# Kernel optimization log

Hardware: AMD Instinct MI355X
Metric: run time of the kernel (lower is better)

The kernel has to match this reference:

```python
import jax, jax.numpy as jnp
import numpy as np

B, N, H, OBS, A = 64, 64, 128, 128, 16
TAU = 0.5
BN = B * N
SQRT_H = float(np.sqrt(H))
_ar = np.arange(N)
# off-diagonal gather indices: row i lists all j != i in increasing order,
# matching torch's eye-mask boolean select in row-major order
IDX = jnp.asarray(np.stack([np.concatenate([_ar[:i], _ar[i + 1:]]) for i in range(N)]))  # [N, N-1]


def setup_inputs() -> dict:
    key = jax.random.key(0)
    ks = jax.random.split(key, 26)
    w = lambda k, s: jax.random.normal(k, s, jnp.float32) * 0.05
    return {
        "obs": jax.random.normal(ks[0], (BN, OBS), jnp.float32),
        "lstm_h": jax.random.normal(ks[1], (BN, 1, H), jnp.float32),
        "lstm_c": jax.random.normal(ks[2], (BN, 1, H), jnp.float32),
        "masks": jnp.ones((BN, 1), jnp.float32),
        "W_enc": w(ks[3], (H, OBS)), "b_enc": jnp.zeros((H,), jnp.float32),
        "lstm_Wih": w(ks[4], (4 * H, H)), "lstm_Whh": w(ks[5], (4 * H, H)),
        "lstm_bih": jnp.zeros((4 * H,), jnp.float32), "lstm_bhh": jnp.zeros((4 * H,), jnp.float32),
        "gru_Wih_f": w(ks[6], (3 * H, 2 * H)), "gru_Whh_f": w(ks[7], (3 * H, H)),
        "gru_bih_f": jnp.zeros((3 * H,), jnp.float32), "gru_bhh_f": jnp.zeros((3 * H,), jnp.float32),
        "gru_Wih_b": w(ks[8], (3 * H, 2 * H)), "gru_Whh_b": w(ks[9], (3 * H, H)),
        "gru_bih_b": jnp.zeros((3 * H,), jnp.float32), "gru_bhh_b": jnp.zeros((3 * H,), jnp.float32),
        "W_hard": w(ks[10], (2, 2 * H)), "b_hard": jnp.zeros((2,), jnp.float32),
        "Wq": w(ks[11], (H, H)), "Wk": w(ks[12], (H, H)),
        "W_act": w(ks[13], (A, 2 * H)), "b_act": jnp.zeros((A,), jnp.float32),
        # fixed Gumbel noise for the gumbel-softmax (makes reference deterministic)
        "gumbel": -jnp.log(-jnp.log(jax.random.uniform(ks[14], (BN, N - 1, 2), jnp.float32, 1e-6, 1.0 - 1e-6))),
    }


def _gru_scan(x_seq, Wih, Whh, bih, bhh):
    # x_seq: [T, BN2, 2H] -> outputs [T, BN2, H]
    def step(hst, x):
        gi = x @ Wih.T + bih
        gh = hst @ Whh.T + bhh
        gi_r, gi_z, gi_n = jnp.split(gi, 3, -1)
        gh_r, gh_z, gh_n = jnp.split(gh, 3, -1)
        r = jax.nn.sigmoid(gi_r + gh_r)
        z = jax.nn.sigmoid(gi_z + gh_z)
        n = jnp.tanh(gi_n + r * gh_n)
        hn = (1.0 - z) * n + z * hst
        return hn, hn
    h0 = jnp.zeros((x_seq.shape[1], Whh.shape[1]), x_seq.dtype)
    _, outs = jax.lax.scan(step, h0, x_seq)
    return outs


def _forward(obs, lstm_h, lstm_c, masks, W_enc, b_enc, lstm_Wih, lstm_Whh, lstm_bih,
             lstm_bhh, gru_Wih_f, gru_Whh_f, gru_bih_f, gru_bhh_f, gru_Wih_b, gru_Whh_b,
             gru_bih_b, gru_bhh_b, W_hard, b_hard, Wq, Wk, W_act, b_act, gumbel):
    # MLP encoder
    h = jax.nn.relu(obs @ W_enc.T + b_enc)                       # [BN, H]
    # single-step LSTM (recurrent_N = 1), mask resets states
    hprev = lstm_h[:, 0] * masks
    cprev = lstm_c[:, 0] * masks
    gates = h @ lstm_Wih.T + lstm_bih + hprev @ lstm_Whh.T + lstm_bhh
    i, f, g, o = jnp.split(gates, 4, -1)
    c_new = jax.nn.sigmoid(f) * cprev + jax.nn.sigmoid(i) * jnp.tanh(g)
    h = jax.nn.sigmoid(o) * jnp.tanh(c_new)                      # [BN, H]
    h_new, c_out = h[:, None, :], c_new[:, None, :]
    hb = h.reshape(B, N, H)
    h_others = hb[:, IDX]                                        # [B, N, N-1, H]
    h_self = jnp.broadcast_to(hb[:, :, None, :], (B, N, N - 1, H))
    h_pair = jnp.concatenate([h_self, h_others], -1).reshape(BN, N - 1, 2 * H)
    # bidirectional GRU over the N-1 "other agents" axis
    xs = jnp.swapaxes(h_pair, 0, 1)                              # [N-1, BN, 2H]
    out_f = _gru_scan(xs, gru_Wih_f, gru_Whh_f, gru_bih_f, gru_bhh_f)
    out_b = _gru_scan(xs[::-1], gru_Wih_b, gru_Whh_b, gru_bih_b, gru_bhh_b)[::-1]
    gru_out = jnp.swapaxes(jnp.concatenate([out_f, out_b], -1), 0, 1)  # [BN, N-1, 2H]
    # hard attention: gumbel-softmax (straight-through), keep channel 1
    logits = gru_out @ W_hard.T + b_hard                         # [BN, N-1, 2]
    y_soft = jax.nn.softmax((logits + gumbel) / TAU, axis=-1)
    y_hard = jax.nn.one_hot(jnp.argmax(y_soft, -1), 2, dtype=y_soft.dtype)
    y = jax.lax.stop_gradient(y_hard - y_soft) + y_soft
    hard_w = y[:, :, 1].reshape(B, N, N - 1, 1)
    # soft attention (manual scaled dot product over other agents)
    q = (h @ Wq.T).reshape(B, N, H)
    k = (h @ Wk.T).reshape(B, N, H)
    k_others = k[:, IDX]                                         # [B, N, N-1, H]
    soft_w = jax.nn.softmax(jnp.einsum('bnh,bnmh->bnm', q, k_others) / SQRT_H, axis=-1)
    x = jnp.sum(h_others * hard_w * soft_w[..., None], axis=2).reshape(BN, H)
    # action head (Discrete, deterministic=True -> argmax)
    act_logits = jnp.concatenate([h, x], -1) @ W_act.T + b_act   # [BN, A]
    logp = jax.nn.log_softmax(act_logits, -1)
    actions = jnp.argmax(act_logits, -1)
    alp = jnp.take_along_axis(logp, actions[:, None], axis=-1)   # [BN, 1]
    return actions[:, None], alp, h_new, c_out


def reference(obs, lstm_h, lstm_c, masks, W_enc, b_enc, lstm_Wih, lstm_Whh, lstm_bih,
              lstm_bhh, gru_Wih_f, gru_Whh_f, gru_bih_f, gru_bhh_f, gru_Wih_b, gru_Whh_b,
              gru_bih_b, gru_bhh_b, W_hard, b_hard, Wq, Wk, W_act, b_act, gumbel):
    return _forward(obs, lstm_h, lstm_c, masks, W_enc, b_enc, lstm_Wih, lstm_Whh,
                    lstm_bih, lstm_bhh, gru_Wih_f, gru_Whh_f, gru_bih_f, gru_bhh_f,
                    gru_Wih_b, gru_Whh_b, gru_bih_b, gru_bhh_b, W_hard, b_hard,
                    Wq, Wk, W_act, b_act, gumbel)
```

## Files before the change

### kernel.cpp

```cpp
#include <hip/hip_runtime.h>
#include <hip/hip_bf16.h>
#include <math.h>

#define BB   64
#define NN   64
#define HH   128
#define OBS_ 128
#define AA   16
#define BN_  4096
#define NM   63
#define G3   384
#define G4   512
#define UVS  1536
#define QKS  256
#define LDSW 136

typedef _Float16 f16x8 __attribute__((ext_vector_type(8)));
typedef float    f32x4 __attribute__((ext_vector_type(4)));

__device__ __forceinline__ float fsig(float x) {
    return __builtin_amdgcn_rcpf(1.0f + __builtin_amdgcn_exp2f(-1.4426950408889634f * x));
}
__device__ __forceinline__ float ftanh(float x) {
    return 1.0f - 2.0f * __builtin_amdgcn_rcpf(1.0f + __builtin_amdgcn_exp2f(2.8853900817779268f * x));
}

__device__ __forceinline__ unsigned short h2u(_Float16 h) {
    union { _Float16 f; unsigned short u; } cv; cv.f = h; return cv.u;
}

template<bool DUAL, bool RELU, bool RMASK>
__global__ __launch_bounds__(256)
void gemm_mfma(const float* __restrict__ A, int lda,
               const float* __restrict__ A2, int lda2,
               const float* __restrict__ rmask,
               const float* __restrict__ Bs0, const float* __restrict__ Bs1,
               const float* __restrict__ Bs2, const float* __restrict__ Bs3,
               const float* __restrict__ Bd, int ldb, int tilesPerSeg,
               const float* __restrict__ bias0, const float* __restrict__ bias1,
               const float* __restrict__ bias2, const float* __restrict__ bias3,
               float* __restrict__ C, int ldc)
{
    __shared__ __align__(16) unsigned short aHi[64][LDSW];
    __shared__ __align__(16) unsigned short aLo[64][LDSW];

    const int t = threadIdx.x;
    const int w = t >> 6, l = t & 63, li = l & 15, lg = l >> 4;
    const int bx = blockIdx.x, by = blockIdx.y;
    const int seg = bx / tilesPerSeg;
    const int cts = (bx % tilesPerSeg) * 64;
    const float* Bseg    = seg == 0 ? Bs0  : seg == 1 ? Bs1  : seg == 2 ? Bs2  : Bs3;
    const float* biasSeg = seg == 0 ? bias0 : seg == 1 ? bias1 : seg == 2 ? bias2 : bias3;
    const int row0 = by * 64;
    const int cl = w * 16 + li;

    f32x4 accA[4], accB[4];
    #pragma unroll
    for (int rt = 0; rt < 4; ++rt) {
        accA[rt] = (f32x4){0.f,0.f,0.f,0.f};
        accB[rt] = (f32x4){0.f,0.f,0.f,0.f};
    }

    const int npass = DUAL ? 2 : 1;
    for (int pass = 0; pass < npass; ++pass) {
        const float* Ap = pass ? A2 : A;
        const int ldap = pass ? lda2 : lda;
        __syncthreads();
        {
            const int ar = t >> 2, kof = (t & 3) * 32;
            const float* src = Ap + (size_t)(row0 + ar) * ldap + kof;
            float mk = 1.0f;
            if (RMASK && pass == 1) mk = rmask[row0 + ar];
            #pragma unroll
            for (int q = 0; q < 8; ++q) {
                float4 v = *(const float4*)(src + q * 4);
                if (RMASK && pass == 1) { v.x *= mk; v.y *= mk; v.z *= mk; v.w *= mk; }
                float vv[4] = {v.x, v.y, v.z, v.w};
                unsigned int hi01, hi23, lo01, lo23;
                {
                    _Float16 h0 = (_Float16)vv[0], h1 = (_Float16)vv[1];
                    _Float16 h2 = (_Float16)vv[2], h3 = (_Float16)vv[3];
                    _Float16 l0 = (_Float16)((vv[0] - (float)h0) * 1024.0f);
                    _Float16 l1 = (_Float16)((vv[1] - (float)h1) * 1024.0f);
                    _Float16 l2 = (_Float16)((vv[2] - (float)h2) * 1024.0f);
                    _Float16 l3 = (_Float16)((vv[3] - (float)h3) * 1024.0f);
                    hi01 = (unsigned int)h2u(h0) | ((unsigned int)h2u(h1) << 16);
                    hi23 = (unsigned int)h2u(h2) | ((unsigned int)h2u(h3) << 16);
                    lo01 = (unsigned int)h2u(l0) | ((unsigned int)h2u(l1) << 16);
                    lo23 = (unsigned int)h2u(l2) | ((unsigned int)h2u(l3) << 16);
                }
                *(uint2*)&aHi[ar][kof + q * 4] = make_uint2(hi01, hi23);
                *(uint2*)&aLo[ar][kof + q * 4] = make_uint2(lo01, lo23);
            }
        }
        const float* Bp = (DUAL && pass) ? Bd : Bseg;
        f16x8 bhi[4], blo[4];
        #pragma unroll
        for (int kt = 0; kt < 4; ++kt) {
            const float* srcB = Bp + (size_t)(cts + cl) * ldb + kt * 32 + lg * 8;
            #pragma unroll
            for (int j = 0; j < 8; ++j) {
                float wv = srcB[j];
                _Float16 hi = (_Float16)wv;
                _Float16 lo = (_Float16)((wv - (float)hi) * 1024.0f);
                bhi[kt][j] = hi;
                blo[kt][j] = lo;
            }
        }
        __syncthreads();
        #pragma unroll
        for (int kt = 0; kt < 4; ++kt) {
            const int koff = kt * 32 + lg * 8;
            #pragma unroll
            for (int rt = 0; rt < 4; ++rt) {
                f16x8 ah = *(const f16x8*)&aHi[rt * 16 + li][koff];
                f16x8 al = *(const f16x8*)&aLo[rt * 16 + li][koff];
                accA[rt] = __builtin_amdgcn_mfma_f32_16x16x32_f16(ah, bhi[kt], accA[rt], 0, 0, 0);
                accB[rt] = __builtin_amdgcn_mfma_f32_16x16x32_f16(al, bhi[kt], accB[rt], 0, 0, 0);
                accB[rt] = __builtin_amdgcn_mfma_f32_16x16x32_f16(ah, blo[kt], accB[rt], 0, 0, 0);
            }
        }
    }

    const float bv = biasSeg ? biasSeg[cts + cl] : 0.0f;
    const int gcol = bx * 64 + cl;
    #pragma unroll
    for (int rt = 0; rt < 4; ++rt)
        #pragma unroll
        for (int rg = 0; rg < 4; ++rg) {
            float x = fmaf(accB[rt][rg], 9.765625e-4f, accA[rt][rg]) + bv;
            if (RELU) x = fmaxf(x, 0.0f);
            const int r = row0 + rt * 16 + lg * 4 + rg;
            C[(size_t)r * ldc + gcol] = x;
        }
}

__global__ void lstm_pointwise(const float* __restrict__ gates,
                               const float* __restrict__ bih, const float* __restrict__ bhh,
                               const float* __restrict__ lstm_c, const float* __restrict__ masks,
                               float* __restrict__ h,
                               float* __restrict__ out_h, float* __restrict__ out_c)
{
    int idx = blockIdx.x * 256 + threadIdx.x;
    int r = idx >> 7, c = idx & 127;
    const float* g = gates + (size_t)r * G4;
    float gi = g[c]        + bih[c]        + bhh[c];
    float gf = g[128 + c]  + bih[128 + c]  + bhh[128 + c];
    float gg = g[256 + c]  + bih[256 + c]  + bhh[256 + c];
    float go = g[384 + c]  + bih[384 + c]  + bhh[384 + c];
    float cprev = lstm_c[idx] * masks[r];
    float cn = fsig(gf) * cprev + fsig(gi) * ftanh(gg);
    float hn = fsig(go) * ftanh(cn);
    h[idx] = hn;
    out_h[idx] = hn;
    out_c[idx] = cn;
}

__global__ __launch_bounds__(512, 2)
void gru_scan(const float* __restrict__ WhhF, const float* __restrict__ WhhB,
              const float* __restrict__ bhhF, const float* __restrict__ bhhB,
              const float* __restrict__ uv,
              const float* __restrict__ Whard,
              float* __restrict__ partF, float* __restrict__ partB)
{
    __shared__ __align__(16) unsigned short hHi[2][32][LDSW];
    __shared__ __align__(16) unsigned short hLo[2][32][LDSW];
    __shared__ float partLds[32][64][2];

    const int t = threadIdx.x;
    const int dir = blockIdx.x >> 7;
    const int blk = blockIdx.x & 127;
    const int r0 = blk * 32;
    const int bbx = r0 >> 6;
    const int n0 = r0 & 63;
    const int w  = t >> 6;
    const int l  = t & 63;
    const int li = l & 15;
    const int lg = l >> 4;
    const int cl = w * 16 + li;
    const bool pw = (w < 2);

    const float* Whh = dir ? WhhB : WhhF;
    const float* bhh = dir ? bhhB : bhhF;
    const float* U   = uv + dir * 768;
    const float* V   = uv + dir * 768 + 384;
    float* part      = dir ? partB : partF;

    f16x8 Bhi[3][4], Blo[3][4];
    #pragma unroll
    for (int g = 0; g < 3; ++g)
        #pragma unroll
        for (int kt = 0; kt < 4; ++kt) {
            const float* src = Whh + (size_t)(g * 128 + cl) * 128 + kt * 32 + lg * 8;
            #pragma unroll
            for (int j = 0; j < 8; ++j) {
                float wv = src[j];
                _Float16 hi = (_Float16)wv;
                _Float16 lo = (_Float16)((wv - (float)hi) * 1024.0f);
                Bhi[g][kt][j] = hi;
                Blo[g][kt][j] = lo;
            }
        }

    f16x8 Phi[4], Plo[4];
    if (pw) {
        #pragma unroll
        for (int kt = 0; kt < 4; ++kt) {
            #pragma unroll
            for (int j = 0; j < 8; ++j) {
                float wv = (li < 2) ? Whard[li * 256 + dir * 128 + kt * 32 + lg * 8 + j] : 0.0f;
                _Float16 hi = (_Float16)wv;
                _Float16 lo = (_Float16)((wv - (float)hi) * 1024.0f);
                Phi[kt][j] = hi;
                Plo[kt][j] = lo;
            }
        }
    }

    const float bh_r = bhh[cl];
    const float bh_z = bhh[128 + cl];
    const float bh_n = bhh[256 + cl];
    float u_r[8], u_z[8], u_n[8];
    #pragma unroll
    for (int rt = 0; rt < 2; ++rt)
        #pragma unroll
        for (int rg = 0; rg < 4; ++rg) {
            const int idx = rt * 4 + rg;
            const int R = r0 + rt * 16 + lg * 4 + rg;
            const float* Ur = U + (size_t)R * UVS;
            u_r[idx] = Ur[cl]       + bh_r;
            u_z[idx] = Ur[128 + cl] + bh_z;
            u_n[idx] = Ur[256 + cl] + bh_n;
        }

    const int vbase = bbx << 6;
    float v0r, v0z, v0n, v1r, v1z, v1n;
    {
        const int tt0 = dir ? (NM - 1) : 0;
        const float* Vr0 = V + (size_t)(vbase + tt0) * UVS;
        const float* Vr1 = V + (size_t)(vbase + tt0 + 1) * UVS;
        v0r = Vr0[cl]; v0z = Vr0[128 + cl]; v0n = Vr0[256 + cl];
        v1r = Vr1[cl]; v1z = Vr1[128 + cl]; v1n = Vr1[256 + cl];
    }

    for (int i = t; i < 2 * 32 * LDSW; i += 512) {
        (&hHi[0][0][0])[i] = 0;
        (&hLo[0][0][0])[i] = 0;
    }
    float hreg[8] = {0.f,0.f,0.f,0.f,0.f,0.f,0.f,0.f};

    int cur = 0;
    __syncthreads();

    for (int s = 0; s < NM; ++s) {
        const int tt = dir ? (NM - 1 - s) : s;

        float p0r, p0z, p0n, p1r, p1z, p1n;
        {
            const int sn = (s + 1 < NM) ? s + 1 : s;
            const int ttn = dir ? (NM - 1 - sn) : sn;
            const float* Vr0 = V + (size_t)(vbase + ttn) * UVS;
            const float* Vr1 = V + (size_t)(vbase + ttn + 1) * UVS;
            p0r = Vr0[cl]; p0z = Vr0[128 + cl]; p0n = Vr0[256 + cl];
            p1r = Vr1[cl]; p1z = Vr1[128 + cl]; p1n = Vr1[256 + cl];
        }

        f32x4 accA[3][2], accB[3][2], pA, pB;
        #pragma unroll
        for (int g = 0; g < 3; ++g)
            #pragma unroll
            for (int rt = 0; rt < 2; ++rt) {
                accA[g][rt] = (f32x4){0.f,0.f,0.f,0.f};
                accB[g][rt] = (f32x4){0.f,0.f,0.f,0.f};
            }
        pA = pB = (f32x4){0.f,0.f,0.f,0.f};

        #pragma unroll
        for (int kt = 0; kt < 4; ++kt) {
            f16x8 Ahi[2], Alo[2];
            const int koff = kt * 32 + lg * 8;
            #pragma unroll
            for (int rt = 0; rt < 2; ++rt) {
                const int arow = rt * 16 + li;
                Ahi[rt] = *(const f16x8*)&hHi[cur][arow][koff];
                Alo[rt] = *(const f16x8*)&hLo[cur][arow][koff];
            }
            #pragma unroll
            for (int g = 0; g < 3; ++g)
                #pragma unroll
                for (int rt = 0; rt < 2; ++rt) {
                    accA[g][rt] = __builtin_amdgcn_mfma_f32_16x16x32_f16(Ahi[rt], Bhi[g][kt], accA[g][rt], 0, 0, 0);
                    accB[g][rt] = __builtin_amdgcn_mfma_f32_16x16x32_f16(Alo[rt], Bhi[g][kt], accB[g][rt], 0, 0, 0);
                    accB[g][rt] = __builtin_amdgcn_mfma_f32_16x16x32_f16(Ahi[rt], Blo[g][kt], accB[g][rt], 0, 0, 0);
                }
            if (pw) {
                const f16x8 Aph = (w == 0) ? Ahi[0] : Ahi[1];
                const f16x8 Apl = (w == 0) ? Alo[0] : Alo[1];
                pA = __builtin_amdgcn_mfma_f32_16x16x32_f16(Aph, Phi[kt], pA, 0, 0, 0);
                pB = __builtin_amdgcn_mfma_f32_16x16x32_f16(Apl, Phi[kt], pB, 0, 0, 0);
                pB = __builtin_amdgcn_mfma_f32_16x16x32_f16(Aph, Plo[kt], pB, 0, 0, 0);
            }
        }

        if (pw && s > 0 && li < 2) {
            const int ttp = dir ? (tt + 1) : (tt - 1);
            #pragma unroll
            for (int rg = 0; rg < 4; ++rg) {
                const int row = w * 16 + lg * 4 + rg;
                partLds[row][ttp][li] = pA[rg] + pB[rg] * 9.765625e-4f;
            }
        }

        #pragma unroll
        for (int rt = 0; rt < 2; ++rt) {
            #pragma unroll
            for (int rg = 0; rg < 4; ++rg) {
                const int idx = rt * 4 + rg;
                const int row = rt * 16 + lg * 4 + rg;
                const int n = n0 + row;
                const bool up = (tt >= n);
                const float vr_ = up ? v1r : v0r;
                const float vz_ = up ? v1z : v0z;
                const float vn_ = up ? v1n : v0n;
                const float gr = fmaf(accB[0][rt][rg], 9.765625e-4f, accA[0][rt][rg]);
                const float gz = fmaf(accB[1][rt][rg], 9.765625e-4f, accA[1][rt][rg]);
                const float gn = fmaf(accB[2][rt][rg], 9.765625e-4f, accA[2][rt][rg]);
                const float rr  = fsig(u_r[idx] + vr_ + gr);
                const float zz  = fsig(u_z[idx] + vz_ + gz);
                const float nn2 = ftanh(u_n[idx] + vn_ + rr * gn);
                hreg[idx] = fmaf(zz, hreg[idx] - nn2, nn2);
            }
        }

        v0r = p0r; v0z = p0z; v0n = p0n;
        v1r = p1r; v1z = p1z; v1n = p1n;

        const int nxt = cur ^ 1;
        #pragma unroll
        for (int rt = 0; rt < 2; ++rt)
            #pragma unroll
            for (int rg = 0; rg < 4; ++rg) {
                const int row = rt * 16 + lg * 4 + rg;
                const float hn = hreg[rt * 4 + rg];
                _Float16 hi = (_Float16)hn;
                _Float16 lo = (_Float16)((hn - (float)hi) * 1024.0f);
                hHi[nxt][row][cl] = h2u(hi);
                hLo[nxt][row][cl] = h2u(lo);
            }
        cur = nxt;
        __syncthreads();
    }

    if (pw) {
        f32x4 qA = (f32x4){0.f,0.f,0.f,0.f}, qB = (f32x4){0.f,0.f,0.f,0.f};
        #pragma unroll
        for (int kt = 0; kt < 4; ++kt) {
            const int koff = kt * 32 + lg * 8;
            f16x8 Ah = *(const f16x8*)&hHi[cur][w * 16 + li][koff];
            f16x8 Al = *(const f16x8*)&hLo[cur][w * 16 + li][koff];
            qA = __builtin_amdgcn_mfma_f32_16x16x32_f16(Ah, Phi[kt], qA, 0, 0, 0);
            qB = __builtin_amdgcn_mfma_f32_16x16x32_f16(Al, Phi[kt], qB, 0, 0, 0);
            qB = __builtin_amdgcn_mfma_f32_16x16x32_f16(Ah, Plo[kt], qB, 0, 0, 0);
        }
        if (li < 2) {
            const int ttl = dir ? 0 : NM - 1;
            #pragma unroll
            for (int rg = 0; rg < 4; ++rg) {
                const int row = w * 16 + lg * 4 + rg;
                partLds[row][ttl][li] = qA[rg] + qB[rg] * 9.765625e-4f;
            }
        }
    }
    __syncthreads();

    {
        const int row = t >> 4;
        const int seg = t & 15;
        float* dst = part + (size_t)(r0 + row) * (NM * 2);
        #pragma unroll
        for (int k = 0; k < 4; ++k) {
            const int m = seg * 4 + k;
            if (m < NM) {
                float2 v = *(const float2*)&partLds[row][m][0];
                *(float2*)&dst[m * 2] = v;
            }
        }
    }
}

__global__ __launch_bounds__(128)
void attn_final(const float* __restrict__ h, const float* __restrict__ qk,
                const float* __restrict__ partF, const float* __restrict__ partB,
                const float* __restrict__ bhard, const float* __restrict__ gum,
                const float* __restrict__ Wact, const float* __restrict__ bact,
                float* __restrict__ out_act, float* __restrict__ out_alp)
{
    const int r = blockIdx.x;
    const int bbx = r >> 6, n = r & 63;
    const int t = threadIdx.x;
    __shared__ float qsh[HH], wsh[NM], shh[HH], shx[HH];
    if (t < HH) { qsh[t] = qk[(size_t)r * QKS + t]; shh[t] = h[(size_t)r * HH + t]; }
    __syncthreads();
    if (t < 64) {
        float sc = -INFINITY;
        float hardv = 0.0f;
        if (t < NM) {
            const int idxm = t + (t >= n ? 1 : 0);
            const float4* kr = (const float4*)(qk + (size_t)((bbx << 6) + idxm) * QKS + 128);
            float s = 0.0f;
            #pragma unroll
            for (int j4 = 0; j4 < 32; ++j4) {
                float4 kv = kr[j4];
                float4 qv = *(const float4*)&qsh[j4 * 4];
                s += kv.x * qv.x + kv.y * qv.y + kv.z * qv.z + kv.w * qv.w;
            }
            sc = s * 0.088388347648318447f;
            const float2 pf = *(const float2*)(partF + ((size_t)r * NM + t) * 2);
            const float2 pb = *(const float2*)(partB + ((size_t)r * NM + t) * 2);
            const float2 gv = *(const float2*)(gum + ((size_t)r * NM + t) * 2);
            const float l0 = pf.x + pb.x + bhard[0] + gv.x;
            const float l1 = pf.y + pb.y + bhard[1] + gv.y;
            hardv = (l1 > l0) ? 1.0f : 0.0f;
        }
        float mx = sc;
        #pragma unroll
        for (int d = 32; d; d >>= 1) mx = fmaxf(mx, __shfl_xor(mx, d, 64));
        const float e = (t < NM) ? expf(sc - mx) : 0.0f;
        float sum = e;
        #pragma unroll
        for (int d = 32; d; d >>= 1) sum += __shfl_xor(sum, d, 64);
        if (t < NM) wsh[t] = hardv * e / sum;
    }
    __syncthreads();
    {
        const int j = t;
        float x = 0.0f;
        for (int m = 0; m < NM; ++m) {
            const int idxm = m + (m >= n ? 1 : 0);
            x = fmaf(wsh[m], h[(size_t)((bbx << 6) + idxm) * HH + j], x);
        }
        shx[j] = x;
    }
    __syncthreads();
    if (t < 16) {
        const float* wa = Wact + (size_t)t * 256;
        float acc = bact[t];
        #pragma unroll
        for (int j4 = 0; j4 < 32; ++j4) {
            float4 w1 = *(const float4*)&wa[j4 * 4];
            float4 hv = *(const float4*)&shh[j4 * 4];
            float4 w2 = *(const float4*)&wa[128 + j4 * 4];
            float4 xv = *(const float4*)&shx[j4 * 4];
            acc += w1.x * hv.x + w1.y * hv.y + w1.z * hv.z + w1.w * hv.w
                 + w2.x * xv.x + w2.y * xv.y + w2.z * xv.z + w2.w * xv.w;
        }
        float mx = acc; int am = t;
        #pragma unroll
        for (int d = 8; d; d >>= 1) {
            const float om = __shfl_xor(mx, d, 16);
            const int   oa = __shfl_xor(am, d, 16);
            if (om > mx || (om == mx && oa < am)) { mx = om; am = oa; }
        }
        const float e = expf(acc - mx);
        float sum = e;
        #pragma unroll
        for (int d = 8; d; d >>= 1) sum += __shfl_xor(sum, d, 16);
        if (t == 0) {
            out_act[r] = (float)am;
            out_alp[r] = -logf(sum);
        }
    }
}

extern "C" void kernel_launch(void* const* d_in, const int* in_sizes, int n_in,
                              void* d_out, int out_size, void* d_ws, size_t ws_size,
                              hipStream_t stream)
{
    const float* obs    = (const float*)d_in[0];
    const float* lstm_h = (const float*)d_in[1];
    const float* lstm_c = (const float*)d_in[2];
    const float* masks  = (const float*)d_in[3];
    const float* W_enc  = (const float*)d_in[4];
    const float* b_enc  = (const float*)d_in[5];
    const float* lWih   = (const float*)d_in[6];
    const float* lWhh   = (const float*)d_in[7];
    const float* lbih   = (const float*)d_in[8];
    const float* lbhh   = (const float*)d_in[9];
    const float* gWihf  = (const float*)d_in[10];
    const float* gWhhf  = (const float*)d_in[11];
    const float* gbihf  = (const float*)d_in[12];
    const float* gbhhf  = (const float*)d_in[13];
    const float* gWihb  = (const float*)d_in[14];
    const float* gWhhb  = (const float*)d_in[15];
    const float* gbihb  = (const float*)d_in[16];
    const float* gbhhb  = (const float*)d_in[17];
    const float* Whard  = (const float*)d_in[18];
    const float* bhard  = (const float*)d_in[19];
    const float* Wq     = (const float*)d_in[20];
    const float* Wk     = (const float*)d_in[21];
    const float* Wact   = (const float*)d_in[22];
    const float* bact   = (const float*)d_in[23];
    const float* gum    = (const float*)d_in[24];

    float* W = (float*)d_ws;
    float* h     = W; W += (size_t)BN_ * HH;
    float* henc  = W; W += (size_t)BN_ * HH;
    float* gates = W; W += (size_t)BN_ * G4;
    float* uv    = W; W += (size_t)BN_ * UVS;
    float* partF = W; W += (size_t)BN_ * NM * 2;
    float* partB = W; W += (size_t)BN_ * NM * 2;
    float* qk    = W; W += (size_t)BN_ * QKS;

    float* out_f   = (float*)d_out;
    float* out_act = out_f;
    float* out_alp = out_act + BN_;
    float* out_h   = out_alp + BN_;
    float* out_c   = out_h + (size_t)BN_ * HH;

    gemm_mfma<false, true, false><<<dim3(2, BN_ / 64), 256, 0, stream>>>(
        obs, OBS_, nullptr, 0, nullptr,
        W_enc, nullptr, nullptr, nullptr, nullptr, OBS_, 2,
        b_enc, nullptr, nullptr, nullptr, henc, HH);
    gemm_mfma<true, false, true><<<dim3(8, BN_ / 64), 256, 0, stream>>>(
        henc, HH, lstm_h, HH, masks,
        lWih, nullptr, nullptr, nullptr, lWhh, HH, 8,
        nullptr, nullptr, nullptr, nullptr, gates, G4);
    lstm_pointwise<<<BN_ * HH / 256, 256, 0, stream>>>(gates, lbih, lbhh, lstm_c, masks,
                                                       h, out_h, out_c);
    gemm_mfma<false, false, false><<<dim3(24, BN_ / 64), 256, 0, stream>>>(
        h, HH, nullptr, 0, nullptr,
        gWihf, gWihf + HH, gWihb, gWihb + HH, nullptr, 2 * HH, 6,
        gbihf, nullptr, gbihb, nullptr, uv, UVS);
    gemm_mfma<false, false, false><<<dim3(4, BN_ / 64), 256, 0, stream>>>(
        h, HH, nullptr, 0, nullptr,
        Wq, Wk, nullptr, nullptr, nullptr, HH, 2,
        nullptr, nullptr, nullptr, nullptr, qk, QKS);
    gru_scan<<<256, 512, 0, stream>>>(gWhhf, gWhhb, gbhhf, gbhhb, uv,
                                      Whard, partF, partB);
    attn_final<<<BN_, 128, 0, stream>>>(h, qk, partF, partB, bhard, gum,
                                        Wact, bact, out_act, out_alp);
}
```

Before: 253.9 us.

## Merge Q/K projection into GRU input GEMM and split scan step into half-tiles

The separate Wq/Wk GEMM launch is folded into the GRU input-projection GEMM by adding two extra weight segments, writing Q/K into a widened shared output buffer. This removes one kernel launch and one extra read of h. The GRU scan step is also restructured to process the two 16-row halves sequentially, writing each half's new hidden state to LDS right after its gate math. That lets the second half's MFMAs overlap the first half's pointwise work and lowers register pressure, at the cost of strided Q/K reads in attn_final.

```diff
diff --git a/kernel.cpp b/kernel.cpp
--- a/kernel.cpp
+++ b/kernel.cpp
@@ -11,8 +11,7 @@
 #define NM   63
 #define G3   384
 #define G4   512
-#define UVS  1536
-#define QKS  256
+#define UVS  1792
 #define LDSW 136
 
 typedef _Float16 f16x8 __attribute__((ext_vector_type(8)));
@@ -36,9 +35,9 @@
                const float* __restrict__ rmask,
                const float* __restrict__ Bs0, const float* __restrict__ Bs1,
                const float* __restrict__ Bs2, const float* __restrict__ Bs3,
-               const float* __restrict__ Bd, int ldb, int tilesPerSeg,
-               const float* __restrict__ bias0, const float* __restrict__ bias1,
-               const float* __restrict__ bias2, const float* __restrict__ bias3,
+               const float* __restrict__ Bs4, const float* __restrict__ Bs5,
+               const float* __restrict__ Bd, int ldb, int ldb2, int tilesPerSeg,
+               const float* __restrict__ bias0, const float* __restrict__ bias2,
                float* __restrict__ C, int ldc)
 {
     __shared__ __align__(16) unsigned short aHi[64][LDSW];
@@ -47,10 +46,14 @@
     const int t = threadIdx.x;
     const int w = t >> 6, l = t & 63, li = l & 15, lg = l >> 4;
     const int bx = blockIdx.x, by = blockIdx.y;
-    const int seg = bx / tilesPerSeg;
-    const int cts = (bx % tilesPerSeg) * 64;
-    const float* Bseg    = seg == 0 ? Bs0  : seg == 1 ? Bs1  : seg == 2 ? Bs2  : Bs3;
-    const float* biasSeg = seg == 0 ? bias0 : seg == 1 ? bias1 : seg == 2 ? bias2 : bias3;
+    int seg, tIdx;
+    if (bx < 4 * tilesPerSeg) { seg = bx / tilesPerSeg; tIdx = bx % tilesPerSeg; }
+    else { const int r2 = bx - 4 * tilesPerSeg; seg = 4 + (r2 >> 1); tIdx = r2 & 1; }
+    const int cts = tIdx * 64;
+    const float* Bseg = seg == 0 ? Bs0 : seg == 1 ? Bs1 : seg == 2 ? Bs2
+                       : seg == 3 ? Bs3 : seg == 4 ? Bs4 : Bs5;
+    const float* biasSeg = seg == 0 ? bias0 : seg == 2 ? bias2 : nullptr;
+    const int ldbs = (seg < 4) ? ldb : ldb2;
     const int row0 = by * 64;
     const int cl = w * 16 + li;
 
@@ -94,10 +97,11 @@
             }
         }
         const float* Bp = (DUAL && pass) ? Bd : Bseg;
+        const int ldbp = (DUAL && pass) ? ldb : ldbs;
         f16x8 bhi[4], blo[4];
         #pragma unroll
         for (int kt = 0; kt < 4; ++kt) {
-            const float* srcB = Bp + (size_t)(cts + cl) * ldb + kt * 32 + lg * 8;
+            const float* srcB = Bp + (size_t)(cts + cl) * ldbp + kt * 32 + lg * 8;
             #pragma unroll
             for (int j = 0; j < 8; ++j) {
                 float wv = srcB[j];
@@ -159,7 +163,7 @@
 __global__ __launch_bounds__(512, 2)
 void gru_scan(const float* __restrict__ WhhF, const float* __restrict__ WhhB,
               const float* __restrict__ bhhF, const float* __restrict__ bhhB,
-              const float* __restrict__ uv,
+              const float* __restrict__ uvqk,
               const float* __restrict__ Whard,
               float* __restrict__ partF, float* __restrict__ partB)
 {
@@ -178,12 +182,11 @@
     const int li = l & 15;
     const int lg = l >> 4;
     const int cl = w * 16 + li;
-    const bool pw = (w < 2);
 
     const float* Whh = dir ? WhhB : WhhF;
     const float* bhh = dir ? bhhB : bhhF;
-    const float* U   = uv + dir * 768;
-    const float* V   = uv + dir * 768 + 384;
+    const float* U   = uvqk + dir * 768;
+    const float* V   = uvqk + dir * 768 + 384;
     float* part      = dir ? partB : partF;
 
     f16x8 Bhi[3][4], Blo[3][4];
@@ -202,6 +205,7 @@
             }
         }
 
+    const bool pw = (w < 2);
     f16x8 Phi[4], Plo[4];
     if (pw) {
         #pragma unroll
@@ -254,6 +258,7 @@
 
     for (int s = 0; s < NM; ++s) {
         const int tt = dir ? (NM - 1 - s) : s;
+        const int nxt = cur ^ 1;
 
         float p0r, p0z, p0n, p1r, p1z, p1n;
         {
@@ -265,88 +270,100 @@
             p1r = Vr1[cl]; p1z = Vr1[128 + cl]; p1n = Vr1[256 + cl];
         }
 
-        f32x4 accA[3][2], accB[3][2], pA, pB;
-        #pragma unroll
-        for (int g = 0; g < 3; ++g)
-            #pragma unroll
-            for (int rt = 0; rt < 2; ++rt) {
-                accA[g][rt] = (f32x4){0.f,0.f,0.f,0.f};
-                accB[g][rt] = (f32x4){0.f,0.f,0.f,0.f};
-            }
+        f32x4 a0[3], b0[3], pA, pB;
+        a0[0] = a0[1] = a0[2] = (f32x4){0.f,0.f,0.f,0.f};
+        b0[0] = b0[1] = b0[2] = (f32x4){0.f,0.f,0.f,0.f};
         pA = pB = (f32x4){0.f,0.f,0.f,0.f};
-
-        #pragma unroll
-        for (int kt = 0; kt < 4; ++kt) {
-            f16x8 Ahi[2], Alo[2];
+        #pragma unroll
+        for (int kt = 0; kt < 4; ++kt) {
             const int koff = kt * 32 + lg * 8;
-            #pragma unroll
-            for (int rt = 0; rt < 2; ++rt) {
-                const int arow = rt * 16 + li;
-                Ahi[rt] = *(const f16x8*)&hHi[cur][arow][koff];
-                Alo[rt] = *(const f16x8*)&hLo[cur][arow][koff];
-            }
-            #pragma unroll
-            for (int g = 0; g < 3; ++g)
-                #pragma unroll
-                for (int rt = 0; rt < 2; ++rt) {
-                    accA[g][rt] = __builtin_amdgcn_mfma_f32_16x16x32_f16(Ahi[rt], Bhi[g][kt], accA[g][rt], 0, 0, 0);
-                    accB[g][rt] = __builtin_amdgcn_mfma_f32_16x16x32_f16(Alo[rt], Bhi[g][kt], accB[g][rt], 0, 0, 0);
-                    accB[g][rt] = __builtin_amdgcn_mfma_f32_16x16x32_f16(Ahi[rt], Blo[g][kt], accB[g][rt], 0, 0, 0);
-                }
-            if (pw) {
-                const f16x8 Aph = (w == 0) ? Ahi[0] : Ahi[1];
-                const f16x8 Apl = (w == 0) ? Alo[0] : Alo[1];
-                pA = __builtin_amdgcn_mfma_f32_16x16x32_f16(Aph, Phi[kt], pA, 0, 0, 0);
-                pB = __builtin_amdgcn_mfma_f32_16x16x32_f16(Apl, Phi[kt], pB, 0, 0, 0);
-                pB = __builtin_amdgcn_mfma_f32_16x16x32_f16(Aph, Plo[kt], pB, 0, 0, 0);
-            }
-        }
-
-        if (pw && s > 0 && li < 2) {
+            f16x8 Ah = *(const f16x8*)&hHi[cur][li][koff];
+            f16x8 Al = *(const f16x8*)&hLo[cur][li][koff];
+            #pragma unroll
+            for (int g = 0; g < 3; ++g) {
+                a0[g] = __builtin_amdgcn_mfma_f32_16x16x32_f16(Ah, Bhi[g][kt], a0[g], 0, 0, 0);
+                b0[g] = __builtin_amdgcn_mfma_f32_16x16x32_f16(Al, Bhi[g][kt], b0[g], 0, 0, 0);
+                b0[g] = __builtin_amdgcn_mfma_f32_16x16x32_f16(Ah, Blo[g][kt], b0[g], 0, 0, 0);
+            }
+            if (w == 0) {
+                pA = __builtin_amdgcn_mfma_f32_16x16x32_f16(Ah, Phi[kt], pA, 0, 0, 0);
+                pB = __builtin_amdgcn_mfma_f32_16x16x32_f16(Al, Phi[kt], pB, 0, 0, 0);
+                pB = __builtin_amdgcn_mfma_f32_16x16x32_f16(Ah, Plo[kt], pB, 0, 0, 0);
+            }
+        }
+        #pragma unroll
+        for (int rg = 0; rg < 4; ++rg) {
+            const int row = lg * 4 + rg;
+            const bool up = (tt >= n0 + row);
+            const float gr = fmaf(b0[0][rg], 9.765625e-4f, a0[0][rg]);
+            const float gz = fmaf(b0[1][rg], 9.765625e-4f, a0[1][rg]);
+            const float gn = fmaf(b0[2][rg], 9.765625e-4f, a0[2][rg]);
+            const float rr  = fsig(u_r[rg] + (up ? v1r : v0r) + gr);
+            const float zz  = fsig(u_z[rg] + (up ? v1z : v0z) + gz);
+            const float nn2 = ftanh(u_n[rg] + (up ? v1n : v0n) + rr * gn);
+            const float hn = fmaf(zz, hreg[rg] - nn2, nn2);
+            hreg[rg] = hn;
+            _Float16 hi = (_Float16)hn;
+            _Float16 lo = (_Float16)((hn - (float)hi) * 1024.0f);
+            hHi[nxt][row][cl] = h2u(hi);
+            hLo[nxt][row][cl] = h2u(lo);
+        }
+        if (w == 0 && s > 0 && li < 2) {
             const int ttp = dir ? (tt + 1) : (tt - 1);
             #pragma unroll
-            for (int rg = 0; rg < 4; ++rg) {
-                const int row = w * 16 + lg * 4 + rg;
-                partLds[row][ttp][li] = pA[rg] + pB[rg] * 9.765625e-4f;
-            }
-        }
-
-        #pragma unroll
-        for (int rt = 0; rt < 2; ++rt) {
-            #pragma unroll
-            for (int rg = 0; rg < 4; ++rg) {
-                const int idx = rt * 4 + rg;
-                const int row = rt * 16 + lg * 4 + rg;
-                const int n = n0 + row;
-                const bool up = (tt >= n);
-                const float vr_ = up ? v1r : v0r;
-                const float vz_ = up ? v1z : v0z;
-                const float vn_ = up ? v1n : v0n;
-                const float gr = fmaf(accB[0][rt][rg], 9.765625e-4f, accA[0][rt][rg]);
-                const float gz = fmaf(accB[1][rt][rg], 9.765625e-4f, accA[1][rt][rg]);
-                const float gn = fmaf(accB[2][rt][rg], 9.765625e-4f, accA[2][rt][rg]);
-                const float rr  = fsig(u_r[idx] + vr_ + gr);
-                const float zz  = fsig(u_z[idx] + vz_ + gz);
-                const float nn2 = ftanh(u_n[idx] + vn_ + rr * gn);
-                hreg[idx] = fmaf(zz, hreg[idx] - nn2, nn2);
-            }
+            for (int rg = 0; rg < 4; ++rg)
+                partLds[lg * 4 + rg][ttp][li] = pA[rg] + pB[rg] * 9.765625e-4f;
+        }
+
+        f32x4 a1[3], b1[3];
+        a1[0] = a1[1] = a1[2] = (f32x4){0.f,0.f,0.f,0.f};
+        b1[0] = b1[1] = b1[2] = (f32x4){0.f,0.f,0.f,0.f};
+        f32x4 qA, qB;
+        qA = qB = (f32x4){0.f,0.f,0.f,0.f};
+        #pragma unroll
+        for (int kt = 0; kt < 4; ++kt) {
+            const int koff = kt * 32 + lg * 8;
+            f16x8 Ah = *(const f16x8*)&hHi[cur][16 + li][koff];
+            f16x8 Al = *(const f16x8*)&hLo[cur][16 + li][koff];
+            #pragma unroll
+            for (int g = 0; g < 3; ++g) {
+                a1[g] = __builtin_amdgcn_mfma_f32_16x16x32_f16(Ah, Bhi[g][kt], a1[g], 0, 0, 0);
+                b1[g] = __builtin_amdgcn_mfma_f32_16x16x32_f16(Al, Bhi[g][kt], b1[g], 0, 0, 0);
+                b1[g] = __builtin_amdgcn_mfma_f32_16x16x32_f16(Ah, Blo[g][kt], b1[g], 0, 0, 0);
+            }
+            if (w == 1) {
+                qA = __builtin_amdgcn_mfma_f32_16x16x32_f16(Ah, Phi[kt], qA, 0, 0, 0);
+                qB = __builtin_amdgcn_mfma_f32_16x16x32_f16(Al, Phi[kt], qB, 0, 0, 0);
+                qB = __builtin_amdgcn_mfma_f32_16x16x32_f16(Ah, Plo[kt], qB, 0, 0, 0);
+            }
+        }
+        #pragma unroll
+        for (int rg = 0; rg < 4; ++rg) {
+            const int row = 16 + lg * 4 + rg;
+            const int idx = 4 + rg;
+            const bool up = (tt >= n0 + row);
+            const float gr = fmaf(b1[0][rg], 9.765625e-4f, a1[0][rg]);
+            const float gz = fmaf(b1[1][rg], 9.765625e-4f, a1[1][rg]);
+            const float gn = fmaf(b1[2][rg], 9.765625e-4f, a1[2][rg]);
+            const float rr  = fsig(u_r[idx] + (up ? v1r : v0r) + gr);
+            const float zz  = fsig(u_z[idx] + (up ? v1z : v0z) + gz);
+            const float nn2 = ftanh(u_n[idx] + (up ? v1n : v0n) + rr * gn);
+            const float hn = fmaf(zz, hreg[idx] - nn2, nn2);
+            hreg[idx] = hn;
+            _Float16 hi = (_Float16)hn;
+            _Float16 lo = (_Float16)((hn - (float)hi) * 1024.0f);
+            hHi[nxt][row][cl] = h2u(hi);
+            hLo[nxt][row][cl] = h2u(lo);
+        }
+        if (w == 1 && s > 0 && li < 2) {
+            const int ttp = dir ? (tt + 1) : (tt - 1);
+            #pragma unroll
+            for (int rg = 0; rg < 4; ++rg)
+                partLds[16 + lg * 4 + rg][ttp][li] = qA[rg] + qB[rg] * 9.765625e-4f;
         }
 
         v0r = p0r; v0z = p0z; v0n = p0n;
         v1r = p1r; v1z = p1z; v1n = p1n;
-
-        const int nxt = cur ^ 1;
-        #pragma unroll
-        for (int rt = 0; rt < 2; ++rt)
-            #pragma unroll
-            for (int rg = 0; rg < 4; ++rg) {
-                const int row = rt * 16 + lg * 4 + rg;
-                const float hn = hreg[rt * 4 + rg];
-                _Float16 hi = (_Float16)hn;
-                _Float16 lo = (_Float16)((hn - (float)hi) * 1024.0f);
-                hHi[nxt][row][cl] = h2u(hi);
-                hLo[nxt][row][cl] = h2u(lo);
-            }
         cur = nxt;
         __syncthreads();
     }
@@ -399,14 +416,14 @@
     const int bbx = r >> 6, n = r & 63;
     const int t = threadIdx.x;
     __shared__ float qsh[HH], wsh[NM], shh[HH], shx[HH];
-    if (t < HH) { qsh[t] = qk[(size_t)r * QKS + t]; shh[t] = h[(size_t)r * HH + t]; }
+    if (t < HH) { qsh[t] = qk[(size_t)r * UVS + t]; shh[t] = h[(size_t)r * HH + t]; }
     __syncthreads();
     if (t < 64) {
         float sc = -INFINITY;
         float hardv = 0.0f;
         if (t < NM) {
             const int idxm = t + (t >= n ? 1 : 0);
-            const float4* kr = (const float4*)(qk + (size_t)((bbx << 6) + idxm) * QKS + 128);
+            const float4* kr = (const float4*)(qk + (size_t)((bbx << 6) + idxm) * UVS + 128);
             float s = 0.0f;
             #pragma unroll
             for (int j4 = 0; j4 < 32; ++j4) {
@@ -506,10 +523,9 @@
     float* h     = W; W += (size_t)BN_ * HH;
     float* henc  = W; W += (size_t)BN_ * HH;
     float* gates = W; W += (size_t)BN_ * G4;
-    float* uv    = W; W += (size_t)BN_ * UVS;
+    float* uvqk  = W; W += (size_t)BN_ * UVS;
     float* partF = W; W += (size_t)BN_ * NM * 2;
     float* partB = W; W += (size_t)BN_ * NM * 2;
-    float* qk    = W; W += (size_t)BN_ * QKS;
 
     float* out_f   = (float*)d_out;
     float* out_act = out_f;
@@ -519,24 +535,20 @@
 
     gemm_mfma<false, true, false><<<dim3(2, BN_ / 64), 256, 0, stream>>>(
         obs, OBS_, nullptr, 0, nullptr,
-        W_enc, nullptr, nullptr, nullptr, nullptr, OBS_, 2,
-        b_enc, nullptr, nullptr, nullptr, henc, HH);
+        W_enc, nullptr, nullptr, nullptr, nullptr, nullptr, nullptr,
+        OBS_, OBS_, 2, b_enc, nullptr, henc, HH);
     gemm_mfma<true, false, true><<<dim3(8, BN_ / 64), 256, 0, stream>>>(
         henc, HH, lstm_h, HH, masks,
-        lWih, nullptr, nullptr, nullptr, lWhh, HH, 8,
-        nullptr, nullptr, nullptr, nullptr, gates, G4);
+        lWih, nullptr, nullptr, nullptr, nullptr, nullptr, lWhh,
+        HH, HH, 8, nullptr, nullptr, gates, G4);
     lstm_pointwise<<<BN_ * HH / 256, 256, 0, stream>>>(gates, lbih, lbhh, lstm_c, masks,
                                                        h, out_h, out_c);
-    gemm_mfma<false, false, false><<<dim3(24, BN_ / 64), 256, 0, stream>>>(
+    gemm_mfma<false, false, false><<<dim3(28, BN_ / 64), 256, 0, stream>>>(
         h, HH, nullptr, 0, nullptr,
-        gWihf, gWihf + HH, gWihb, gWihb + HH, nullptr, 2 * HH, 6,
-        gbihf, nullptr, gbihb, nullptr, uv, UVS);
-    gemm_mfma<false, false, false><<<dim3(4, BN_ / 64), 256, 0, stream>>>(
-        h, HH, nullptr, 0, nullptr,
-        Wq, Wk, nullptr, nullptr, nullptr, HH, 2,
-        nullptr, nullptr, nullptr, nullptr, qk, QKS);
-    gru_scan<<<256, 512, 0, stream>>>(gWhhf, gWhhb, gbhhf, gbhhb, uv,
+        gWihf, gWihf + HH, gWihb, gWihb + HH, Wq, Wk, nullptr,
+        2 * HH, HH, 6, gbihf, gbihb, uvqk, UVS);
+    gru_scan<<<256, 512, 0, stream>>>(gWhhf, gWhhb, gbhhf, gbhhb, uvqk,
                                       Whard, partF, partB);
-    attn_final<<<BN_, 128, 0, stream>>>(h, qk, partF, partB, bhard, gum,
+    attn_final<<<BN_, 128, 0, stream>>>(h, uvqk + 1536, partF, partB, bhard, gum,
                                         Wact, bact, out_act, out_alp);
 }
```

Result: faster. 232.0 us, median of 2 (-8.6%).
